# Optimization experiments

Hardware: AMD Instinct MI355X
Metric: run time of the kernel (lower is better)

The kernel has to match this reference:

```python
import jax, jax.numpy as jnp
import numpy as np

B, C_IN, T = 16, 1, 10240
C = 256                # conv_dim_out == config.model.conv_channels
KERNEL, STRIDE, PAD = 10, 5, 0
K_STEPS = 12           # config.model.predict_steps
NEG = 10               # config.train.neg_samples
EPS = 1e-5
L_OUT = (T + 2 * PAD - KERNEL) // STRIDE + 1   # 2047


def setup_inputs() -> dict:
    key = jax.random.key(0)
    ks = jax.random.split(key, 5)
    return {
        "x": jax.random.normal(ks[0], (B, C_IN, T), jnp.float32),
        "conv_w": jax.random.normal(ks[1], (C, C_IN, KERNEL), jnp.float32) * 0.1,
        "conv_b": jnp.zeros((C,), jnp.float32),
        "bn_gamma": jnp.ones((C,), jnp.float32),
        "bn_beta": jnp.zeros((C,), jnp.float32),
        "tr_w": jax.random.normal(ks[2], (K_STEPS, C, C), jnp.float32) / np.sqrt(C).astype(np.float32),
        "tr_b": jnp.zeros((K_STEPS, C), jnp.float32),
        "perm": jax.random.permutation(ks[3], L_OUT),  # randperm over the time axis
    }


def reference(x, conv_w, conv_b, bn_gamma, bn_beta, tr_w, tr_b, perm):
    # ---- encoder: Conv1d -> ReLU -> BatchNorm1d (training-mode batch stats) ----
    h = jax.lax.conv_general_dilated(
        x, conv_w, window_strides=(STRIDE,), padding=[(PAD, PAD)],
        dimension_numbers=("NCH", "OIH", "NCH"))
    h = jax.nn.relu(h + conv_b[None, :, None])            # (B, C, L)
    mu = h.mean(axis=(0, 2), keepdims=True)
    var = h.var(axis=(0, 2), keepdims=True)               # biased, as torch BN
    h = (h - mu) * jax.lax.rsqrt(var + EPS)
    h = h * bn_gamma[None, :, None] + bn_beta[None, :, None]
    z = h.transpose(0, 2, 1)                              # (B, L, C)

    # ---- negatives: batch-roll by 1, random permutation of the time axis; detached ----
    z_negative = jax.lax.stop_gradient(jnp.roll(z, 1, axis=0)[:, perm, :])

    L = z.shape[1]
    # z_neg_full[b, i] == roll(z_neg, i, axis=0)[b] == z_neg[(b - i) % B]
    roll_idx = (jnp.arange(B)[:, None] - jnp.arange(NEG)[None, :]) % B  # (B, NEG)

    losses = []
    for k in range(1, K_STEPS + 1):
        l_len = L - k
        z_pos = z[:, k:, :]                               # (B, l, C)
        z_neg = z_negative[:, k:, :]                      # (B, l, C)
        z_neg_full = z_neg[roll_idx]                      # (B, NEG, l, C)
        W, bb = tr_w[k - 1], tr_b[k - 1]
        est_pos = (z_pos @ W + bb)[:, None]               # (B, 1, l, C)
        est_neg = z_neg_full @ W + bb                     # (B, NEG, l, C)
        estimated = jnp.concatenate([est_pos, est_neg], axis=1)        # (B, S, l, C)
        z_full = jnp.concatenate([z_pos[:, None], z_neg_full], axis=1)  # (B, S, l, C)
        f = jnp.einsum("bslc,bslc->bsl", estimated, z_full)
        # faithful to torch: flatten (b, s, l) row-major then view as (b*l, S)
        f_k = f.reshape(B * l_len, NEG + 1)
        logp = jax.nn.log_softmax(f_k, axis=1)
        losses.append(-logp.sum() / ((l_len - k) * B))

    # torch forward returns z.permute(0, 2, 1); losses returned too for baseline use
    return z.transpose(0, 2, 1), jnp.stack(losses)
```

## Files before the change

kernel.cpp:

```cpp
#include <hip/hip_runtime.h>
#include <hip/hip_bf16.h>
#include <math.h>

constexpr int B_ = 16;
constexpr int T_ = 10240;
constexpr int C_ = 256;
constexpr int KW = 10;
constexpr int L_ = 2047;
constexpr int N_ = B_ * L_;
constexpr int KSTEPS = 12;
constexpr float EPS_ = 1e-5f;
constexpr int QSTR = 32768;

typedef short bf16x8 __attribute__((ext_vector_type(8)));
typedef float f32x4  __attribute__((ext_vector_type(4)));

__global__ __launch_bounds__(256) void stats_wt_kernel(
    const float* __restrict__ x, const float* __restrict__ cw, const float* __restrict__ cb,
    float* __restrict__ ssum, float* __restrict__ ssq,
    const float* __restrict__ tw, __hip_bfloat16* __restrict__ Wt)
{
    __shared__ float smem[64 * 65];
    const int bid = blockIdx.x;
    if (bid < 256) {
        const int b  = bid & 15;
        const int l0 = (bid >> 4) * 128;
        const int c  = threadIdx.x;
        float w[KW];
#pragma unroll
        for (int j = 0; j < KW; ++j) w[j] = cw[c * KW + j];
        const float bias = cb[c];
        const float* xg = x + (size_t)b * T_ + l0 * 5;
        const int xlim = 10236 - 5 * l0;
        float s = 0.f, s2 = 0.f;
        for (int ci = 0; ci < 16; ++ci) {
            float xr[48];
#pragma unroll
            for (int u = 0; u < 12; ++u) {
                int o = min(40 * ci + 4 * u, xlim);
                *(float4*)&xr[u * 4] = *(const float4*)(xg + o);
            }
#pragma unroll
            for (int i = 0; i < 8; ++i) {
                int l = l0 + ci * 8 + i;
                float v = bias;
#pragma unroll
                for (int j = 0; j < KW; ++j) v = fmaf(xr[5 * i + j], w[j], v);
                v = fmaxf(v, 0.f);
                if (l < L_) { s += v; s2 = fmaf(v, v, s2); }
            }
        }
        atomicAdd(&ssum[c], s);
        atomicAdd(&ssq[c], s2);
    } else {
        const int idx = bid - 256;
        const int k  = idx >> 4;
        const int c0 = ((idx & 15) >> 2) * 64, j0 = (idx & 3) * 64;
        float (*tile)[65] = (float(*)[65])smem;
        for (int i = threadIdx.x; i < 64 * 64; i += 256) {
            int c = i >> 6, j = i & 63;
            tile[c][j] = tw[((size_t)k * C_ + (c0 + c)) * C_ + j0 + j];
        }
        __syncthreads();
        for (int i = threadIdx.x; i < 64 * 64; i += 256) {
            int j = i >> 6, c = i & 63;
            Wt[((size_t)k * C_ + (j0 + j)) * C_ + c0 + c] = __float2bfloat16(tile[c][j]);
        }
    }
}

__global__ __launch_bounds__(256) void conv_norm_kernel(
    const float* __restrict__ x, const float* __restrict__ cw, const float* __restrict__ cb,
    const float* __restrict__ ssum, const float* __restrict__ ssq,
    const float* __restrict__ gamma, const float* __restrict__ beta,
    __hip_bfloat16* __restrict__ Zb, float* __restrict__ out0)
{
    const int b  = blockIdx.y;
    const int l0 = blockIdx.x * 32;
    const int c  = threadIdx.x;
    __shared__ float zt2[256][33];

    float w[KW];
#pragma unroll
    for (int j = 0; j < KW; ++j) w[j] = cw[c * KW + j];
    const float bias = cb[c];
    const float inv_n = 1.0f / (float)N_;
    const float mu  = ssum[c] * inv_n;
    const float var = ssq[c] * inv_n - mu * mu;
    const float sc  = gamma[c] * rsqrtf(var + EPS_);
    const float sh  = beta[c] - mu * sc;

    const float* xg = x + (size_t)b * T_ + l0 * 5;
    const int xlim = 10236 - 5 * l0;
#pragma unroll
    for (int ci = 0; ci < 4; ++ci) {
        float xr[48];
#pragma unroll
        for (int u = 0; u < 12; ++u) {
            int o = min(40 * ci + 4 * u, xlim);
            *(float4*)&xr[u * 4] = *(const float4*)(xg + o);
        }
#pragma unroll
        for (int i = 0; i < 8; ++i) {
            int l = l0 + ci * 8 + i;
            float v = bias;
#pragma unroll
            for (int j = 0; j < KW; ++j) v = fmaf(xr[5 * i + j], w[j], v);
            v = fmaxf(v, 0.f);
            float z = fmaf(v, sc, sh);
            if (l < L_) Zb[((size_t)(b * L_ + l)) * C_ + c] = __float2bfloat16(z);
            zt2[c][ci * 8 + i] = z;
        }
    }
    __syncthreads();
    const int q4 = threadIdx.x & 7;
    const int cb0 = threadIdx.x >> 3;
    const int lb = l0 + q4 * 4;
#pragma unroll
    for (int i = 0; i < 8; ++i) {
        int cr = cb0 + 32 * i;
        float4 v;
        v.x = zt2[cr][q4 * 4 + 0];
        v.y = zt2[cr][q4 * 4 + 1];
        v.z = zt2[cr][q4 * 4 + 2];
        v.w = zt2[cr][q4 * 4 + 3];
        float* op = out0 + ((size_t)(b * C_ + cr)) * L_ + lb;
        if (lb + 3 < L_) *(float4*)op = v;
        else {
            if (lb     < L_) op[0] = v.x;
            if (lb + 1 < L_) op[1] = v.y;
            if (lb + 2 < L_) op[2] = v.z;
        }
    }
}

__global__ __launch_bounds__(256, 2) void qmfma_kernel(
    const __hip_bfloat16* __restrict__ Zb, const __hip_bfloat16* __restrict__ Wt,
    const float* __restrict__ tb, float* __restrict__ qt)
{
    const int k   = blockIdx.y;
    const int grp = blockIdx.x;
    const __hip_bfloat16* __restrict__ Wk = Wt + (size_t)k * C_ * C_;

    __shared__ __hip_bfloat16 zs[2][32 * 256];
    __shared__ float qacc[4][128];

    const int tid  = threadIdx.x;
    const int lane = tid & 63, wave = tid >> 6;
    const int n16  = lane & 15, quad = lane >> 4;
    const int sw   = n16 & 7;

    bf16x8 wfrag[4][8];
    {
        const __hip_bfloat16* wb = Wk + ((size_t)(64 * wave + n16)) * C_ + quad * 8;
#pragma unroll
        for (int ct = 0; ct < 4; ++ct)
#pragma unroll
            for (int it = 0; it < 8; ++it)
                wfrag[ct][it] = *(const bf16x8*)(wb + ct * 16 * C_ + it * 32);
    }
    float4 bias4[4];
#pragma unroll
    for (int ct = 0; ct < 4; ++ct)
        bias4[ct] = *(const float4*)(tb + k * C_ + 64 * wave + ct * 16 + quad * 4);

    const int row0 = grp * 128;
    float4 greg[4];

#pragma unroll
    for (int i = 0; i < 4; ++i) {
        int chunk = tid + i * 256;
        int r = chunk >> 5;
        int rg = row0 + r; if (rg > N_ - 1) rg = N_ - 1;
        greg[i] = *(const float4*)(Zb + (size_t)rg * C_ + (chunk & 31) * 8);
    }
#pragma unroll
    for (int i = 0; i < 4; ++i) {
        int chunk = tid + i * 256;
        int r = chunk >> 5, j = chunk & 31;
        *(float4*)((__hip_bfloat16*)zs[0] + r * 256 + (j ^ (r & 7)) * 8) = greg[i];
    }
    __syncthreads();

    for (int t = 0; t < 4; ++t) {
        const int p = t & 1;

        if (t < 3) {
            int r0 = row0 + (t + 1) * 32;
#pragma unroll
            for (int i = 0; i < 4; ++i) {
                int chunk = tid + i * 256;
                int r = chunk >> 5;
                int rg = r0 + r; if (rg > N_ - 1) rg = N_ - 1;
                greg[i] = *(const float4*)(Zb + (size_t)rg * C_ + (chunk & 31) * 8);
            }
        }

        f32x4 acc[2][4];
#pragma unroll
        for (int rt = 0; rt < 2; ++rt)
#pragma unroll
            for (int ct = 0; ct < 4; ++ct) acc[rt][ct] = f32x4{0.f, 0.f, 0.f, 0.f};

        const __hip_bfloat16* zsp = (const __hip_bfloat16*)zs[p];
#pragma unroll
        for (int it = 0; it < 8; ++it) {
            const int js = (it * 4 + quad) ^ sw;
            bf16x8 zf0 = *(const bf16x8*)(zsp + n16 * 256 + js * 8);
            bf16x8 zf1 = *(const bf16x8*)(zsp + (n16 + 16) * 256 + js * 8);
#pragma unroll
            for (int ct = 0; ct < 4; ++ct) {
                acc[0][ct] = __builtin_amdgcn_mfma_f32_16x16x32_bf16(
                    wfrag[ct][it], zf0, acc[0][ct], 0, 0, 0);
                acc[1][ct] = __builtin_amdgcn_mfma_f32_16x16x32_bf16(
                    wfrag[ct][it], zf1, acc[1][ct], 0, 0, 0);
            }
        }

#pragma unroll
        for (int rt = 0; rt < 2; ++rt) {
            const int row = rt * 16 + n16;
            float s = 0.f;
#pragma unroll
            for (int ct = 0; ct < 4; ++ct) {
                const int j  = 8 * wave + 2 * ct + (quad >> 1);
                const char* zp = (const char*)zsp + row * 512 + ((j ^ sw) << 4) + (quad & 1) * 8;
                uint2 zz = *(const uint2*)zp;
                float z0 = __uint_as_float(zz.x << 16);
                float z1 = __uint_as_float(zz.x & 0xffff0000u);
                float z2 = __uint_as_float(zz.y << 16);
                float z3 = __uint_as_float(zz.y & 0xffff0000u);
                s = fmaf(acc[rt][ct][0] + bias4[ct].x, z0, s);
                s = fmaf(acc[rt][ct][1] + bias4[ct].y, z1, s);
                s = fmaf(acc[rt][ct][2] + bias4[ct].z, z2, s);
                s = fmaf(acc[rt][ct][3] + bias4[ct].w, z3, s);
            }
            s += __shfl_xor(s, 16);
            s += __shfl_xor(s, 32);
            if (lane < 16) qacc[wave][t * 32 + row] = s;
        }

        if (t < 3) {
#pragma unroll
            for (int i = 0; i < 4; ++i) {
                int chunk = tid + i * 256;
                int r = chunk >> 5, j = chunk & 31;
                *(float4*)((__hip_bfloat16*)zs[1 - p] + r * 256 + (j ^ (r & 7)) * 8) = greg[i];
            }
        }
        __syncthreads();
    }

    if (tid < 128) {
        int rg = row0 + tid;
        if (rg < N_) {
            float qv = qacc[0][tid] + qacc[1][tid] + qacc[2][tid] + qacc[3][tid];
            int b = rg / L_;
            int l = rg - b * L_;
            qt[(size_t)k * QSTR + (l << 4) + b] = qv;
        }
    }
}

__global__ __launch_bounds__(256) void loss_kernel(
    const float* __restrict__ qt, const int* __restrict__ perm, float* __restrict__ lacc)
{
    const int k = blockIdx.y + 1;
    const float* qk = qt + (size_t)(k - 1) * QSTR;
    const int nval = B_ * (L_ - k);
    const int idx = blockIdx.x * 256 + threadIdx.x;

    float contrib = 0.f;
    if (idx < nval) {
        int b = idx & 15;
        int l = k + (idx >> 4);
        float f0 = qk[(l << 4) | b];
        int pl = perm[l];
        const float* qn = qk + ((size_t)pl << 4);
        float f[10];
#pragma unroll
        for (int n = 0; n < 10; ++n) f[n] = qn[(b + 15 - n) & 15];
        float m = f0;
#pragma unroll
        for (int i = 0; i < 10; ++i) m = fmaxf(m, f[i]);
        float se = expf(f0 - m), fs = f0;
#pragma unroll
        for (int i = 0; i < 10; ++i) { se += expf(f[i] - m); fs += f[i]; }
        contrib = 11.f * (m + logf(se)) - fs;
    }

    __shared__ float red[4];
#pragma unroll
    for (int off = 32; off > 0; off >>= 1) contrib += __shfl_down(contrib, off);
    const int lane = threadIdx.x & 63;
    const int wave = threadIdx.x >> 6;
    if (lane == 0) red[wave] = contrib;
    __syncthreads();
    if (threadIdx.x == 0) atomicAdd(&lacc[k - 1], red[0] + red[1] + red[2] + red[3]);
}

__global__ void finalize_loss_kernel(const float* __restrict__ lacc, float* __restrict__ out1)
{
    int k = threadIdx.x;
    if (k < KSTEPS) {
        float div = (float)((L_ - 2 * (k + 1)) * B_);
        out1[k] = lacc[k] / div;
    }
}

extern "C" void kernel_launch(void* const* d_in, const int* in_sizes, int n_in,
                              void* d_out, int out_size, void* d_ws, size_t ws_size,
                              hipStream_t stream)
{
    const float* x     = (const float*)d_in[0];
    const float* cw    = (const float*)d_in[1];
    const float* cb    = (const float*)d_in[2];
    const float* gamma = (const float*)d_in[3];
    const float* beta  = (const float*)d_in[4];
    const float* tw    = (const float*)d_in[5];
    const float* tb    = (const float*)d_in[6];
    const int*   perm  = (const int*)d_in[7];

    float* out0 = (float*)d_out;
    float* out1 = out0 + (size_t)B_ * C_ * L_;

    char* ws = (char*)d_ws;
    __hip_bfloat16* Zb = (__hip_bfloat16*)ws;   ws += (size_t)N_ * C_ * 2;
    __hip_bfloat16* Wt = (__hip_bfloat16*)ws;   ws += (size_t)KSTEPS * C_ * C_ * 2;
    float* qt    = (float*)ws;                  ws += (size_t)KSTEPS * QSTR * 4;
    float* ssum  = (float*)ws;                  ws += C_ * 4;
    float* ssq   = (float*)ws;                  ws += C_ * 4;
    float* lacc  = (float*)ws;                  ws += 64 * 4;

    hipMemsetAsync(ssum, 0, (C_ + C_ + 64) * sizeof(float), stream);

    stats_wt_kernel<<<448, 256, 0, stream>>>(x, cw, cb, ssum, ssq, tw, Wt);

    dim3 gcv(64, 16);
    conv_norm_kernel<<<gcv, 256, 0, stream>>>(x, cw, cb, ssum, ssq, gamma, beta, Zb, out0);

    dim3 gq(256, KSTEPS);
    qmfma_kernel<<<gq, 256, 0, stream>>>(Zb, Wt, tb, qt);

    dim3 gl(128, KSTEPS);
    loss_kernel<<<gl, 256, 0, stream>>>(qt, perm, lacc);
    finalize_loss_kernel<<<1, 64, 0, stream>>>(lacc, out1);
}
```

Measured before the change: 213.5 us.

## Single-buffer qmfma tiles with higher occupancy, larger row groups, and rework conv transpose store

Result: slower. 355.4 us (+66.5%).

```diff
diff --git a/kernel.cpp b/kernel.cpp
--- a/kernel.cpp
+++ b/kernel.cpp
@@ -78,7 +78,7 @@
     const int b  = blockIdx.y;
     const int l0 = blockIdx.x * 32;
     const int c  = threadIdx.x;
-    __shared__ float zt2[256][33];
+    __shared__ float zt[32][257];
 
     float w[KW];
 #pragma unroll
@@ -109,32 +109,22 @@
             v = fmaxf(v, 0.f);
             float z = fmaf(v, sc, sh);
             if (l < L_) Zb[((size_t)(b * L_ + l)) * C_ + c] = __float2bfloat16(z);
-            zt2[c][ci * 8 + i] = z;
+            zt[ci * 8 + i][c] = z;
         }
     }
     __syncthreads();
-    const int q4 = threadIdx.x & 7;
-    const int cb0 = threadIdx.x >> 3;
-    const int lb = l0 + q4 * 4;
-#pragma unroll
-    for (int i = 0; i < 8; ++i) {
-        int cr = cb0 + 32 * i;
-        float4 v;
-        v.x = zt2[cr][q4 * 4 + 0];
-        v.y = zt2[cr][q4 * 4 + 1];
-        v.z = zt2[cr][q4 * 4 + 2];
-        v.w = zt2[cr][q4 * 4 + 3];
-        float* op = out0 + ((size_t)(b * C_ + cr)) * L_ + lb;
-        if (lb + 3 < L_) *(float4*)op = v;
-        else {
-            if (lb     < L_) op[0] = v.x;
-            if (lb + 1 < L_) op[1] = v.y;
-            if (lb + 2 < L_) op[2] = v.z;
-        }
-    }
-}
-
-__global__ __launch_bounds__(256, 2) void qmfma_kernel(
+    const int lq  = threadIdx.x & 31;
+    const int cr0 = threadIdx.x >> 5;
+    if (l0 + lq < L_) {
+#pragma unroll
+        for (int i = 0; i < 32; ++i) {
+            int cr = cr0 * 32 + i;
+            out0[((size_t)(b * C_ + cr)) * L_ + l0 + lq] = zt[lq][cr];
+        }
+    }
+}
+
+__global__ __launch_bounds__(256, 4) void qmfma_kernel(
     const __hip_bfloat16* __restrict__ Zb, const __hip_bfloat16* __restrict__ Wt,
     const float* __restrict__ tb, float* __restrict__ qt)
 {
@@ -142,8 +132,8 @@
     const int grp = blockIdx.x;
     const __hip_bfloat16* __restrict__ Wk = Wt + (size_t)k * C_ * C_;
 
-    __shared__ __hip_bfloat16 zs[2][32 * 256];
-    __shared__ float qacc[4][128];
+    __shared__ __hip_bfloat16 zs[32 * 256];
+    __shared__ float qacc[4][256];
 
     const int tid  = threadIdx.x;
     const int lane = tid & 63, wave = tid >> 6;
@@ -164,37 +154,19 @@
     for (int ct = 0; ct < 4; ++ct)
         bias4[ct] = *(const float4*)(tb + k * C_ + 64 * wave + ct * 16 + quad * 4);
 
-    const int row0 = grp * 128;
-    float4 greg[4];
-
-#pragma unroll
-    for (int i = 0; i < 4; ++i) {
-        int chunk = tid + i * 256;
-        int r = chunk >> 5;
-        int rg = row0 + r; if (rg > N_ - 1) rg = N_ - 1;
-        greg[i] = *(const float4*)(Zb + (size_t)rg * C_ + (chunk & 31) * 8);
-    }
-#pragma unroll
-    for (int i = 0; i < 4; ++i) {
-        int chunk = tid + i * 256;
-        int r = chunk >> 5, j = chunk & 31;
-        *(float4*)((__hip_bfloat16*)zs[0] + r * 256 + (j ^ (r & 7)) * 8) = greg[i];
-    }
-    __syncthreads();
-
-    for (int t = 0; t < 4; ++t) {
-        const int p = t & 1;
-
-        if (t < 3) {
-            int r0 = row0 + (t + 1) * 32;
-#pragma unroll
-            for (int i = 0; i < 4; ++i) {
-                int chunk = tid + i * 256;
-                int r = chunk >> 5;
-                int rg = r0 + r; if (rg > N_ - 1) rg = N_ - 1;
-                greg[i] = *(const float4*)(Zb + (size_t)rg * C_ + (chunk & 31) * 8);
-            }
-        }
+    const int row0 = grp * 256;
+
+    for (int t = 0; t < 8; ++t) {
+        __syncthreads();
+#pragma unroll
+        for (int i = 0; i < 4; ++i) {
+            int chunk = tid + i * 256;
+            int r = chunk >> 5, j = chunk & 31;
+            int rg = row0 + t * 32 + r; if (rg > N_ - 1) rg = N_ - 1;
+            float4 v = *(const float4*)(Zb + (size_t)rg * C_ + j * 8);
+            *(float4*)(zs + r * 256 + (j ^ (r & 7)) * 8) = v;
+        }
+        __syncthreads();
 
         f32x4 acc[2][4];
 #pragma unroll
@@ -202,12 +174,11 @@
 #pragma unroll
             for (int ct = 0; ct < 4; ++ct) acc[rt][ct] = f32x4{0.f, 0.f, 0.f, 0.f};
 
-        const __hip_bfloat16* zsp = (const __hip_bfloat16*)zs[p];
 #pragma unroll
         for (int it = 0; it < 8; ++it) {
             const int js = (it * 4 + quad) ^ sw;
-            bf16x8 zf0 = *(const bf16x8*)(zsp + n16 * 256 + js * 8);
-            bf16x8 zf1 = *(const bf16x8*)(zsp + (n16 + 16) * 256 + js * 8);
+            bf16x8 zf0 = *(const bf16x8*)(zs + n16 * 256 + js * 8);
+            bf16x8 zf1 = *(const bf16x8*)(zs + (n16 + 16) * 256 + js * 8);
 #pragma unroll
             for (int ct = 0; ct < 4; ++ct) {
                 acc[0][ct] = __builtin_amdgcn_mfma_f32_16x16x32_bf16(
@@ -224,7 +195,7 @@
 #pragma unroll
             for (int ct = 0; ct < 4; ++ct) {
                 const int j  = 8 * wave + 2 * ct + (quad >> 1);
-                const char* zp = (const char*)zsp + row * 512 + ((j ^ sw) << 4) + (quad & 1) * 8;
+                const char* zp = (const char*)zs + row * 512 + ((j ^ sw) << 4) + (quad & 1) * 8;
                 uint2 zz = *(const uint2*)zp;
                 float z0 = __uint_as_float(zz.x << 16);
                 float z1 = __uint_as_float(zz.x & 0xffff0000u);
@@ -239,19 +210,10 @@
             s += __shfl_xor(s, 32);
             if (lane < 16) qacc[wave][t * 32 + row] = s;
         }
-
-        if (t < 3) {
-#pragma unroll
-            for (int i = 0; i < 4; ++i) {
-                int chunk = tid + i * 256;
-                int r = chunk >> 5, j = chunk & 31;
-                *(float4*)((__hip_bfloat16*)zs[1 - p] + r * 256 + (j ^ (r & 7)) * 8) = greg[i];
-            }
-        }
-        __syncthreads();
-    }
-
-    if (tid < 128) {
+    }
+    __syncthreads();
+
+    {
         int rg = row0 + tid;
         if (rg < N_) {
             float qv = qacc[0][tid] + qacc[1][tid] + qacc[2][tid] + qacc[3][tid];
@@ -339,7 +301,7 @@
     dim3 gcv(64, 16);
     conv_norm_kernel<<<gcv, 256, 0, stream>>>(x, cw, cb, ssum, ssq, gamma, beta, Zb, out0);
 
-    dim3 gq(256, KSTEPS);
+    dim3 gq(128, KSTEPS);
     qmfma_kernel<<<gq, 256, 0, stream>>>(Zb, Wt, tb, qt);
 
     dim3 gl(128, KSTEPS);
```
